# Performance work log

Measured on AMD Instinct MI355X. Metric: run time of the kernel, lower is better.

The kernel has to match this reference:

```python
import jax, jax.numpy as jnp
import numpy as np

EMBED = 512
HEADS = 8
DIM_HEAD = 64
SCALE = DIM_HEAD ** -0.5


def setup_inputs() -> dict:
    key = jax.random.key(0)
    k1, k2, k3 = jax.random.split(key, 3)
    x = jax.random.normal(k1, (1, EMBED, 64, 64), dtype=jnp.float32)
    # nn.Linear(embed, 3*embed) weight [out, in] -> store transposed [in, out] for x @ W
    W_qkv = jax.random.normal(k2, (EMBED, 3 * EMBED), dtype=jnp.float32) * (EMBED ** -0.5)
    b_qkv = jax.random.normal(k3, (3 * EMBED,), dtype=jnp.float32) * 0.01
    return {"x": x, "W_qkv": W_qkv, "b_qkv": b_qkv}


def reference(x, W_qkv, b_qkv):
    B, E, h, w = x.shape
    N = h * w
    # [B, E, H, W] -> [B, N, E]
    xs = x.reshape(B, E, N).transpose(0, 2, 1)
    qkv = xs @ W_qkv + b_qkv                      # [B, N, 3E]
    q, k, v = jnp.split(qkv, 3, axis=-1)          # each [B, N, E]

    def heads(t):
        return t.reshape(B, N, HEADS, DIM_HEAD).transpose(0, 2, 1, 3)  # [B, H, N, dh]

    q, k, v = heads(q), heads(k), heads(v)
    # raw (non-softmax) attention scores, materialized as in the original
    attn = jnp.einsum('bhqd,bhkd->bhqk', q, k) * SCALE  # [B, H, N, N]
    coarse_attn = attn.sum(axis=-2)                     # sum over queries -> [B, H, N]
    output = jnp.einsum('bhqk,bhkd->bhqd', attn, v)     # [B, H, N, dh]
    return coarse_attn, output
```

## Files before the change

kernel.cpp:

```cpp
#include <hip/hip_runtime.h>


#define N_TOK 4096
#define EMBED 512
#define J3    1536
#define HEADS 8
#define DH    64
#define SCALE 0.125f

typedef float  floatx4  __attribute__((ext_vector_type(4)));
typedef short  shortx8  __attribute__((ext_vector_type(8)));
typedef unsigned short ushortx4 __attribute__((ext_vector_type(4)));
typedef unsigned int u32;
typedef unsigned short ushort;

__device__ inline ushort f2bf(float f) {
    union { float f; u32 u; } x; x.f = f;
    u32 r = x.u + 0x7fffu + ((x.u >> 16) & 1u);
    return (ushort)(r >> 16);
}
__device__ inline float bf2f(ushort u) {
    union { u32 u; float f; } x; x.u = ((u32)u) << 16; return x.f;
}
__device__ static inline void async_copy16(void* lds, const void* g) {
    auto* gp = (const __attribute__((address_space(1))) u32*)g;
    auto* lp = (__attribute__((address_space(3))) u32*)lds;
    __builtin_amdgcn_global_load_lds(gp, lp, 16, 0, 0);
}
__device__ inline int permj(int j) {
    if (j < 512) return j;
    if (j < 1024) return 512 + ((j - 512) >> 6) * 128 + ((j - 512) & 63);
    return 512 + ((j - 1024) >> 6) * 128 + 64 + ((j - 1024) & 63);
}

__global__ __launch_bounds__(256) void prep(const float* __restrict__ x,
                                            const float* __restrict__ W,
                                            ushort* __restrict__ xT,
                                            ushort* __restrict__ WT,
                                            float* __restrict__ xsum) {
    const int t = threadIdx.x;
    int bx = blockIdx.x;
    const bool isx = bx < 64;
    const float* src = isx ? x : W;
    const int C = isx ? N_TOK : J3;
    if (!isx) bx -= 64;
    __shared__ float T[64][65];
    __shared__ float red[256];
    const int c0 = bx * 64, r0 = blockIdx.y * 64;
    #pragma unroll
    for (int k = 0; k < 16; ++k) {
        int i = t + 256 * k; int r = i >> 6, c = i & 63;
        T[r][c] = src[(size_t)(r0 + r) * C + c0 + c];
    }
    __syncthreads();
    if (isx) {
        int row = t >> 2, seg = (t & 3) * 16;
        float s = 0.f;
        #pragma unroll
        for (int cc = 0; cc < 16; ++cc) s += T[row][seg + cc];
        red[t] = s;
    }
    #pragma unroll
    for (int k = 0; k < 4; ++k) {
        int i = t + 256 * k; int cr = i >> 4, cc4 = (i & 15) * 4;
        ushortx4 o = { f2bf(T[cc4 + 0][cr]), f2bf(T[cc4 + 1][cr]),
                       f2bf(T[cc4 + 2][cr]), f2bf(T[cc4 + 3][cr]) };
        int dr = isx ? (c0 + cr) : permj(c0 + cr);
        ushort* dst = isx ? xT : WT;
        *(ushortx4*)&dst[(size_t)dr * 512 + r0 + cc4] = o;
    }
    if (isx) {
        __syncthreads();
        if ((t & 3) == 0)
            atomicAdd(&xsum[r0 + (t >> 2)], red[t] + red[t + 1] + red[t + 2] + red[t + 3]);
    }
}

__global__ __launch_bounds__(256) void qkv_m(const ushort* __restrict__ xT,
                                             const ushort* __restrict__ WT,
                                             const float* __restrict__ bias,
                                             const float* __restrict__ xsum,
                                             ushort* __restrict__ Qb,
                                             float* __restrict__ Mp,
                                             float* __restrict__ out) {
    const int bx = blockIdx.x, ch = blockIdx.y;
    const int j0 = bx * 128, n0 = ch * 64;
    const bool iskv = bx >= 4;
    const int h = bx - 4;
    __shared__ __align__(16) char lds[18432];
    short* As = (short*)lds;
    short* Bs = (short*)(lds + 4096);
    short* Kt = (short*)lds;
    short* Vt = (short*)(lds + 9216);
    short* Qt = (short*)lds;
    __shared__ float cred[64 * 33];
    __shared__ float qs[64];
    const int t = threadIdx.x, lane = t & 63, w = t >> 6;
    const int quad = lane >> 4, mrow = lane & 15;

    if (iskv) {
        int jl = t >> 2, seg = (t & 3) * 128;
        const ushort* wr = WT + (size_t)(h * 64 + jl) * 512 + seg;
        float qa = 0.f;
        #pragma unroll
        for (int g = 0; g < 16; ++g) {
            shortx8 wv = *(const shortx8*)(wr + g * 8);
            #pragma unroll
            for (int u = 0; u < 8; ++u)
                qa += bf2f((ushort)wv[u]) * xsum[seg + g * 8 + u];
        }
        cred[t] = qa;
        __syncthreads();
        if (t < 64)
            qs[t] = 4096.f * bias[h * 64 + t]
                  + cred[4 * t] + cred[4 * t + 1] + cred[4 * t + 2] + cred[4 * t + 3];
    }

    floatx4 acc[4][2] = {};
    for (int e0 = 0; e0 < 512; e0 += 32) {
        __syncthreads();
        {
            int row = t >> 2, q = t & 3;
            async_copy16((char*)As + (size_t)w * 1024,
                         xT + (size_t)(n0 + row) * 512 + e0 + q * 8);
        }
        #pragma unroll
        for (int s = 0; s < 2; ++s) {
            int i = t + 256 * s; int row = i >> 2, q = i & 3;
            async_copy16((char*)Bs + (size_t)w * 1024 + (size_t)s * 4096,
                         WT + (size_t)(j0 + row) * 512 + e0 + q * 8);
        }
        __syncthreads();
        shortx8 a[4], b[2];
        #pragma unroll
        for (int mi = 0; mi < 4; ++mi)
            a[mi] = *(const shortx8*)&As[(mi * 16 + mrow) * 32 + quad * 8];
        #pragma unroll
        for (int ni = 0; ni < 2; ++ni)
            b[ni] = *(const shortx8*)&Bs[(w * 32 + ni * 16 + mrow) * 32 + quad * 8];
        #pragma unroll
        for (int mi = 0; mi < 4; ++mi)
            #pragma unroll
            for (int ni = 0; ni < 2; ++ni)
                acc[mi][ni] = __builtin_amdgcn_mfma_f32_16x16x32_bf16(a[mi], b[ni], acc[mi][ni], 0, 0, 0);
    }
    __syncthreads();

    if (!iskv) {
        #pragma unroll
        for (int ni = 0; ni < 2; ++ni) {
            int cl = w * 32 + ni * 16 + mrow;
            float bj = bias[j0 + cl];
            #pragma unroll
            for (int mi = 0; mi < 4; ++mi)
                #pragma unroll
                for (int r = 0; r < 4; ++r) {
                    int tok = mi * 16 + quad * 4 + r;
                    Qt[tok * 136 + cl] = (short)f2bf(acc[mi][ni][r] + bj);
                }
        }
        __syncthreads();
        #pragma unroll
        for (int k = 0; k < 4; ++k) {
            int u = t + 256 * k; int row = u >> 4, seg = u & 15;
            *(shortx8*)(Qb + (size_t)(n0 + row) * 512 + j0 + seg * 8) =
                *(const shortx8*)&Qt[row * 136 + seg * 8];
        }
        return;
    }

    {
        short* dst = (w < 2) ? Kt : Vt;
        const int dhb = (w & 1) * 32;
        const int boff = (w < 2) ? 512 : 1024;
        float cp[16] = {};
        #pragma unroll
        for (int ni = 0; ni < 2; ++ni) {
            int dh = dhb + ni * 16 + mrow;
            float bj = bias[boff + h * 64 + dh];
            float qv = qs[dh];
            #pragma unroll
            for (int mi = 0; mi < 4; ++mi)
                #pragma unroll
                for (int r = 0; r < 4; ++r) {
                    int tok = mi * 16 + quad * 4 + r;
                    float v = acc[mi][ni][r] + bj;
                    dst[dh * 72 + tok] = (short)f2bf(v);
                    if (w < 2) cp[mi * 4 + r] += v * qv;
                }
        }
        if (w < 2) {
            #pragma unroll
            for (int mi = 0; mi < 4; ++mi)
                #pragma unroll
                for (int r = 0; r < 4; ++r)
                    cred[(mi * 16 + quad * 4 + r) * 33 + w * 16 + mrow] = cp[mi * 4 + r];
        }
    }
    __syncthreads();
    const int dpb = (w & 1) * 32, db = (w >> 1) * 32;
    floatx4 m[2][2] = {};
    #pragma unroll
    for (int kt = 0; kt < 2; ++kt) {
        shortx8 ka[2], vb[2];
        #pragma unroll
        for (int fi = 0; fi < 2; ++fi)
            ka[fi] = *(const shortx8*)&Kt[(dpb + fi * 16 + mrow) * 72 + kt * 32 + quad * 8];
        #pragma unroll
        for (int fj = 0; fj < 2; ++fj)
            vb[fj] = *(const shortx8*)&Vt[(db + fj * 16 + mrow) * 72 + kt * 32 + quad * 8];
        #pragma unroll
        for (int fi = 0; fi < 2; ++fi)
            #pragma unroll
            for (int fj = 0; fj < 2; ++fj)
                m[fi][fj] = __builtin_amdgcn_mfma_f32_16x16x32_bf16(ka[fi], vb[fj], m[fi][fj], 0, 0, 0);
    }
    float* mp = Mp + ((size_t)h * 64 + ch) * 4096;
    #pragma unroll
    for (int fi = 0; fi < 2; ++fi)
        #pragma unroll
        for (int fj = 0; fj < 2; ++fj)
            #pragma unroll
            for (int r = 0; r < 4; ++r)
                mp[(dpb + fi * 16 + quad * 4 + r) * 64 + db + fj * 16 + mrow] = m[fi][fj][r];
    if (t < 64) {
        float s = 0.f;
        #pragma unroll
        for (int c = 0; c < 32; ++c) s += cred[t * 33 + c];
        out[h * N_TOK + n0 + t] = s * SCALE;
    }
}

__global__ __launch_bounds__(256) void reduce_m(const float* __restrict__ Mp,
                                                ushort* __restrict__ Mt) {
    const int h = blockIdx.x, part = blockIdx.y;
    const int t = threadIdx.x;
    __shared__ float sh[4][64];
    float s = 0.f;
    for (int c = 0; c < 64; ++c)
        s += Mp[((size_t)h * 64 + c) * 4096 + part * 256 + t];
    sh[t >> 6][t & 63] = s;
    __syncthreads();
    if (t < 64) {
        ushortx4 o = { f2bf(sh[0][t]), f2bf(sh[1][t]), f2bf(sh[2][t]), f2bf(sh[3][t]) };
        *(ushortx4*)&Mt[(size_t)h * 4096 + t * 64 + part * 4] = o;
    }
}

__global__ __launch_bounds__(256) void out_kernel(const ushort* __restrict__ Qb,
                                                  const ushort* __restrict__ Mt,
                                                  float* __restrict__ out) {
    const int h = blockIdx.x, n0 = blockIdx.y * 64;
    const int t = threadIdx.x, lane = t & 63, w = t >> 6;
    const int quad = lane >> 4, mrow = lane & 15;
    __shared__ float Os[64 * 68];
    floatx4 acc[4] = {};
    #pragma unroll
    for (int ks = 0; ks < 2; ++ks) {
        shortx8 a = *(const shortx8*)(Qb + (size_t)(n0 + w * 16 + mrow) * 512 + h * DH + ks * 32 + quad * 8);
        #pragma unroll
        for (int ni = 0; ni < 4; ++ni) {
            shortx8 b = *(const shortx8*)(Mt + (size_t)h * 4096 + (ni * 16 + mrow) * 64 + ks * 32 + quad * 8);
            acc[ni] = __builtin_amdgcn_mfma_f32_16x16x32_bf16(a, b, acc[ni], 0, 0, 0);
        }
    }
    #pragma unroll
    for (int ni = 0; ni < 4; ++ni)
        #pragma unroll
        for (int r = 0; r < 4; ++r)
            Os[(w * 16 + quad * 4 + r) * 68 + ni * 16 + mrow] = acc[ni][r] * SCALE;
    __syncthreads();
    float* op = out + HEADS * N_TOK + (size_t)h * N_TOK * DH + (size_t)n0 * DH;
    #pragma unroll
    for (int k = 0; k < 4; ++k) {
        int u = t + 256 * k; int row = u >> 4, seg = u & 15;
        *(floatx4*)(op + row * 64 + seg * 4) = *(const floatx4*)&Os[row * 68 + seg * 4];
    }
}

extern "C" void kernel_launch(void* const* d_in, const int* in_sizes, int n_in,
                              void* d_out, int out_size, void* d_ws, size_t ws_size,
                              hipStream_t stream) {
    const float* x = (const float*)d_in[0];
    const float* W = (const float*)d_in[1];
    const float* b = (const float*)d_in[2];
    float* out = (float*)d_out;

    ushort* xT = (ushort*)d_ws;
    ushort* WT = xT + (size_t)N_TOK * EMBED;
    ushort* Qb = WT + (size_t)J3 * EMBED;
    ushort* Mt = Qb + (size_t)N_TOK * EMBED;
    float* Mp   = (float*)(Mt + (size_t)HEADS * DH * DH);
    float* xsum = Mp + (size_t)HEADS * 64 * 4096;

    prep<<<dim3(88, 8), 256, 0, stream>>>(x, W, xT, WT, xsum);
    qkv_m<<<dim3(12, 64), 256, 0, stream>>>(xT, WT, b, xsum, Qb, Mp, out);
    reduce_m<<<dim3(8, 16), 256, 0, stream>>>(Mp, Mt);
    out_kernel<<<dim3(8, 64), 256, 0, stream>>>(Qb, Mt, out);
}
```

Baseline: 106.9 us.

## Enlarge QKV GEMM tile to 128x128 with K=64 steps and single-wave output kernel

The QKV projection kernel now computes 128-token by 128-column tiles, with each wave holding a 64x64 accumulator block, and loads K in chunks of 64. This halves the number of blocks, the partial K^T V matrices and the reduction work, and improves operand reuse per LDS load. The output kernel is rewritten to use one wave per block and to write results directly from registers instead of staging them in LDS. The risks are higher LDS use and register pressure, which lower occupancy, a grid of only 384 blocks for many CUs, and less coalesced direct output stores.

```diff
diff --git a/kernel.cpp b/kernel.cpp
--- a/kernel.cpp
+++ b/kernel.cpp
@@ -84,18 +84,19 @@
                                              float* __restrict__ Mp,
                                              float* __restrict__ out) {
     const int bx = blockIdx.x, ch = blockIdx.y;
-    const int j0 = bx * 128, n0 = ch * 64;
+    const int j0 = bx * 128, n0 = ch * 128;
     const bool iskv = bx >= 4;
     const int h = bx - 4;
-    __shared__ __align__(16) char lds[18432];
+    __shared__ __align__(16) char lds[34816];
     short* As = (short*)lds;
-    short* Bs = (short*)(lds + 4096);
+    short* Bs = (short*)(lds + 16384);
     short* Kt = (short*)lds;
-    short* Vt = (short*)(lds + 9216);
+    short* Vt = (short*)(lds + 17408);
     short* Qt = (short*)lds;
-    __shared__ float cred[64 * 33];
+    __shared__ float cred[128 * 17];
     __shared__ float qs[64];
     const int t = threadIdx.x, lane = t & 63, w = t >> 6;
+    const int wm = w & 1, wn = w >> 1;
     const int quad = lane >> 4, mrow = lane & 15;
 
     if (iskv) {
@@ -116,52 +117,53 @@
                   + cred[4 * t] + cred[4 * t + 1] + cred[4 * t + 2] + cred[4 * t + 3];
     }
 
-    floatx4 acc[4][2] = {};
-    for (int e0 = 0; e0 < 512; e0 += 32) {
-        __syncthreads();
-        {
-            int row = t >> 2, q = t & 3;
-            async_copy16((char*)As + (size_t)w * 1024,
+    floatx4 acc[4][4] = {};
+    for (int e0 = 0; e0 < 512; e0 += 64) {
+        __syncthreads();
+        #pragma unroll
+        for (int s = 0; s < 4; ++s) {
+            int i = t + 256 * s;
+            int row = i >> 3, q = i & 7;
+            async_copy16((char*)As + ((size_t)w * 64 + 256 * s) * 16,
                          xT + (size_t)(n0 + row) * 512 + e0 + q * 8);
-        }
-        #pragma unroll
-        for (int s = 0; s < 2; ++s) {
-            int i = t + 256 * s; int row = i >> 2, q = i & 3;
-            async_copy16((char*)Bs + (size_t)w * 1024 + (size_t)s * 4096,
+            async_copy16((char*)Bs + ((size_t)w * 64 + 256 * s) * 16,
                          WT + (size_t)(j0 + row) * 512 + e0 + q * 8);
         }
         __syncthreads();
-        shortx8 a[4], b[2];
-        #pragma unroll
-        for (int mi = 0; mi < 4; ++mi)
-            a[mi] = *(const shortx8*)&As[(mi * 16 + mrow) * 32 + quad * 8];
-        #pragma unroll
-        for (int ni = 0; ni < 2; ++ni)
-            b[ni] = *(const shortx8*)&Bs[(w * 32 + ni * 16 + mrow) * 32 + quad * 8];
-        #pragma unroll
-        for (int mi = 0; mi < 4; ++mi)
-            #pragma unroll
-            for (int ni = 0; ni < 2; ++ni)
-                acc[mi][ni] = __builtin_amdgcn_mfma_f32_16x16x32_bf16(a[mi], b[ni], acc[mi][ni], 0, 0, 0);
+        #pragma unroll
+        for (int kk = 0; kk < 2; ++kk) {
+            shortx8 a[4], b[4];
+            #pragma unroll
+            for (int mi = 0; mi < 4; ++mi)
+                a[mi] = *(const shortx8*)&As[(wm * 64 + mi * 16 + mrow) * 64 + kk * 32 + quad * 8];
+            #pragma unroll
+            for (int ni = 0; ni < 4; ++ni)
+                b[ni] = *(const shortx8*)&Bs[(wn * 64 + ni * 16 + mrow) * 64 + kk * 32 + quad * 8];
+            #pragma unroll
+            for (int mi = 0; mi < 4; ++mi)
+                #pragma unroll
+                for (int ni = 0; ni < 4; ++ni)
+                    acc[mi][ni] = __builtin_amdgcn_mfma_f32_16x16x32_bf16(a[mi], b[ni], acc[mi][ni], 0, 0, 0);
+        }
     }
     __syncthreads();
 
     if (!iskv) {
         #pragma unroll
-        for (int ni = 0; ni < 2; ++ni) {
-            int cl = w * 32 + ni * 16 + mrow;
+        for (int ni = 0; ni < 4; ++ni) {
+            int cl = wn * 64 + ni * 16 + mrow;
             float bj = bias[j0 + cl];
             #pragma unroll
             for (int mi = 0; mi < 4; ++mi)
                 #pragma unroll
                 for (int r = 0; r < 4; ++r) {
-                    int tok = mi * 16 + quad * 4 + r;
+                    int tok = wm * 64 + mi * 16 + quad * 4 + r;
                     Qt[tok * 136 + cl] = (short)f2bf(acc[mi][ni][r] + bj);
                 }
         }
         __syncthreads();
         #pragma unroll
-        for (int k = 0; k < 4; ++k) {
+        for (int k = 0; k < 8; ++k) {
             int u = t + 256 * k; int row = u >> 4, seg = u & 15;
             *(shortx8*)(Qb + (size_t)(n0 + row) * 512 + j0 + seg * 8) =
                 *(const shortx8*)&Qt[row * 136 + seg * 8];
@@ -170,52 +172,51 @@
     }
 
     {
-        short* dst = (w < 2) ? Kt : Vt;
-        const int dhb = (w & 1) * 32;
-        const int boff = (w < 2) ? 512 : 1024;
+        short* dst = (wn == 0) ? Kt : Vt;
+        const int boff = (wn == 0) ? 512 : 1024;
         float cp[16] = {};
         #pragma unroll
-        for (int ni = 0; ni < 2; ++ni) {
-            int dh = dhb + ni * 16 + mrow;
+        for (int ni = 0; ni < 4; ++ni) {
+            int dh = ni * 16 + mrow;
             float bj = bias[boff + h * 64 + dh];
             float qv = qs[dh];
             #pragma unroll
             for (int mi = 0; mi < 4; ++mi)
                 #pragma unroll
                 for (int r = 0; r < 4; ++r) {
-                    int tok = mi * 16 + quad * 4 + r;
+                    int tok = wm * 64 + mi * 16 + quad * 4 + r;
                     float v = acc[mi][ni][r] + bj;
-                    dst[dh * 72 + tok] = (short)f2bf(v);
-                    if (w < 2) cp[mi * 4 + r] += v * qv;
+                    dst[dh * 136 + tok] = (short)f2bf(v);
+                    if (wn == 0) cp[mi * 4 + r] += v * qv;
                 }
         }
-        if (w < 2) {
+        if (wn == 0) {
             #pragma unroll
             for (int mi = 0; mi < 4; ++mi)
                 #pragma unroll
                 for (int r = 0; r < 4; ++r)
-                    cred[(mi * 16 + quad * 4 + r) * 33 + w * 16 + mrow] = cp[mi * 4 + r];
+                    cred[(wm * 64 + mi * 16 + quad * 4 + r) * 17 + mrow] = cp[mi * 4 + r];
         }
     }
     __syncthreads();
     const int dpb = (w & 1) * 32, db = (w >> 1) * 32;
     floatx4 m[2][2] = {};
     #pragma unroll
-    for (int kt = 0; kt < 2; ++kt) {
+    for (int kt = 0; kt < 4; ++kt) {
         shortx8 ka[2], vb[2];
         #pragma unroll
         for (int fi = 0; fi < 2; ++fi)
-            ka[fi] = *(const shortx8*)&Kt[(dpb + fi * 16 + mrow) * 72 + kt * 32 + quad * 8];
+            ka[fi] = *(const shortx8*)&Kt[(dpb + fi * 16 + mrow) * 136 + kt * 32 + quad * 8];
         #pragma unroll
         for (int fj = 0; fj < 2; ++fj)
-            vb[fj] = *(const shortx8*)&Vt[(db + fj * 16 + mrow) * 72 + kt * 32 + quad * 8];
+            vb[fj] = *(const shortx8*)&Vt[(db + fj * 16 + mrow) * 136 + kt * 32 + quad * 8];
         #pragma unroll
         for (int fi = 0; fi < 2; ++fi)
             #pragma unroll
             for (int fj = 0; fj < 2; ++fj)
                 m[fi][fj] = __builtin_amdgcn_mfma_f32_16x16x32_bf16(ka[fi], vb[fj], m[fi][fj], 0, 0, 0);
     }
-    float* mp = Mp + ((size_t)h * 64 + ch) * 4096;
+    float* mp = Mp + ((size_t)h * 32 + ch) * 4096;
     #pragma unroll
     for (int fi = 0; fi < 2; ++fi)
         #pragma unroll
@@ -223,10 +224,10 @@
             #pragma unroll
             for (int r = 0; r < 4; ++r)
                 mp[(dpb + fi * 16 + quad * 4 + r) * 64 + db + fj * 16 + mrow] = m[fi][fj][r];
-    if (t < 64) {
+    if (t < 128) {
         float s = 0.f;
         #pragma unroll
-        for (int c = 0; c < 32; ++c) s += cred[t * 33 + c];
+        for (int c = 0; c < 16; ++c) s += cred[t * 17 + c];
         out[h * N_TOK + n0 + t] = s * SCALE;
     }
 }
@@ -237,8 +238,8 @@
     const int t = threadIdx.x;
     __shared__ float sh[4][64];
     float s = 0.f;
-    for (int c = 0; c < 64; ++c)
-        s += Mp[((size_t)h * 64 + c) * 4096 + part * 256 + t];
+    for (int c = 0; c < 32; ++c)
+        s += Mp[((size_t)h * 32 + c) * 4096 + part * 256 + t];
     sh[t >> 6][t & 63] = s;
     __syncthreads();
     if (t < 64) {
@@ -247,35 +248,38 @@
     }
 }
 
-__global__ __launch_bounds__(256) void out_kernel(const ushort* __restrict__ Qb,
-                                                  const ushort* __restrict__ Mt,
-                                                  float* __restrict__ out) {
+__global__ __launch_bounds__(64) void out_kernel(const ushort* __restrict__ Qb,
+                                                 const ushort* __restrict__ Mt,
+                                                 float* __restrict__ out) {
     const int h = blockIdx.x, n0 = blockIdx.y * 64;
-    const int t = threadIdx.x, lane = t & 63, w = t >> 6;
+    const int lane = threadIdx.x;
     const int quad = lane >> 4, mrow = lane & 15;
-    __shared__ float Os[64 * 68];
-    floatx4 acc[4] = {};
+    floatx4 acc[4][4] = {};
     #pragma unroll
     for (int ks = 0; ks < 2; ++ks) {
-        shortx8 a = *(const shortx8*)(Qb + (size_t)(n0 + w * 16 + mrow) * 512 + h * DH + ks * 32 + quad * 8);
-        #pragma unroll
-        for (int ni = 0; ni < 4; ++ni) {
-            shortx8 b = *(const shortx8*)(Mt + (size_t)h * 4096 + (ni * 16 + mrow) * 64 + ks * 32 + quad * 8);
-            acc[ni] = __builtin_amdgcn_mfma_f32_16x16x32_bf16(a, b, acc[ni], 0, 0, 0);
-        }
-    }
-    #pragma unroll
-    for (int ni = 0; ni < 4; ++ni)
-        #pragma unroll
-        for (int r = 0; r < 4; ++r)
-            Os[(w * 16 + quad * 4 + r) * 68 + ni * 16 + mrow] = acc[ni][r] * SCALE;
-    __syncthreads();
-    float* op = out + HEADS * N_TOK + (size_t)h * N_TOK * DH + (size_t)n0 * DH;
-    #pragma unroll
-    for (int k = 0; k < 4; ++k) {
-        int u = t + 256 * k; int row = u >> 4, seg = u & 15;
-        *(floatx4*)(op + row * 64 + seg * 4) = *(const floatx4*)&Os[row * 68 + seg * 4];
-    }
+        shortx8 a[4], b[4];
+        #pragma unroll
+        for (int mi = 0; mi < 4; ++mi)
+            a[mi] = *(const shortx8*)(Qb + (size_t)(n0 + mi * 16 + mrow) * 512 + h * DH + ks * 32 + quad * 8);
+        #pragma unroll
+        for (int ni = 0; ni < 4; ++ni)
+            b[ni] = *(const shortx8*)(Mt + (size_t)h * 4096 + (ni * 16 + mrow) * 64 + ks * 32 + quad * 8);
+        #pragma unroll
+        for (int mi = 0; mi < 4; ++mi)
+            #pragma unroll
+            for (int ni = 0; ni < 4; ++ni)
+                acc[mi][ni] = __builtin_amdgcn_mfma_f32_16x16x32_bf16(a[mi], b[ni], acc[mi][ni], 0, 0, 0);
+    }
+    float* op = out + HEADS * N_TOK + (size_t)h * N_TOK * DH;
+    #pragma unroll
+    for (int mi = 0; mi < 4; ++mi)
+        #pragma unroll
+        for (int r = 0; r < 4; ++r) {
+            int n = n0 + mi * 16 + quad * 4 + r;
+            #pragma unroll
+            for (int ni = 0; ni < 4; ++ni)
+                op[(size_t)n * DH + ni * 16 + mrow] = acc[mi][ni][r] * SCALE;
+        }
 }
 
 extern "C" void kernel_launch(void* const* d_in, const int* in_sizes, int n_in,
@@ -291,10 +295,10 @@
     ushort* Qb = WT + (size_t)J3 * EMBED;
     ushort* Mt = Qb + (size_t)N_TOK * EMBED;
     float* Mp   = (float*)(Mt + (size_t)HEADS * DH * DH);
-    float* xsum = Mp + (size_t)HEADS * 64 * 4096;
+    float* xsum = Mp + (size_t)HEADS * 32 * 4096;
 
     prep<<<dim3(88, 8), 256, 0, stream>>>(x, W, xT, WT, xsum);
-    qkv_m<<<dim3(12, 64), 256, 0, stream>>>(xT, WT, b, xsum, Qb, Mp, out);
+    qkv_m<<<dim3(12, 32), 256, 0, stream>>>(xT, WT, b, xsum, Qb, Mp, out);
     reduce_m<<<dim3(8, 16), 256, 0, stream>>>(Mp, Mt);
-    out_kernel<<<dim3(8, 64), 256, 0, stream>>>(Qb, Mt, out);
-}
+    out_kernel<<<dim3(8, 64), 64, 0, stream>>>(Qb, Mt, out);
+}
```

New measurement: 103.7 us. -3.0%, faster.
